# Kernel optimization log

Measured on AMD Instinct MI355X. Metric: run time of the kernel, lower is better.

The kernel has to match this reference:

```python
import jax, jax.numpy as jnp
import numpy as np
from jax import lax

B, S, H = 2, 2048, 768
FF = 1536
E = 8
TOP_K = 2


def setup_inputs() -> dict:
    key = jax.random.key(0)
    k1, k2, k3, k4 = jax.random.split(key, 4)
    hidden_states = jax.random.normal(k1, (B, S, H), dtype=jnp.float32)
    # torch init: weight.normal_() for experts; nn.Linear default init for gate (approx normal here is fine for a numerics baseline)
    gate_w = jax.random.normal(k2, (E, H), dtype=jnp.float32) * 0.02
    w_fc = jax.random.normal(k3, (E, FF, H), dtype=jnp.float32) * 0.02
    w_proj = jax.random.normal(k4, (E, H, FF), dtype=jnp.float32) * 0.02
    return {"hidden_states": hidden_states, "gate_w": gate_w, "w_fc": w_fc, "w_proj": w_proj}


def reference(hidden_states, gate_w, w_fc, w_proj):
    b, s, h = hidden_states.shape
    x = hidden_states.reshape(-1, h)                      # [T, H]
    # --- top-k gating (logits in float32, as in the torch code) ---
    logits = (x @ gate_w.T).astype(jnp.float32)           # [T, E]
    top_logits, top_idx = lax.top_k(logits, TOP_K)        # [T, K]
    gates = jax.nn.softmax(top_logits, axis=1).astype(x.dtype)  # [T, K]
    # combined per-token/per-expert gate: g[t,e] = sum_k gates[t,k]*[idx[t,k]==e]
    onehot = jax.nn.one_hot(top_idx, E, dtype=x.dtype)    # [T, K, E]
    g = jnp.einsum('tk,tke->te', gates, onehot)           # [T, E]
    # --- experts: gather + per-expert GEMM + gated scatter-add combine ---
    # Equivalent math: tokens with zero gate for expert e contribute nothing,
    # so compute each expert on all tokens and weight by g[:, e].
    out = jnp.zeros_like(x)
    for e in range(E):  # fixed small loop over experts (structurally distinct weights)
        hmid = jax.nn.gelu(x @ w_fc[e].T, approximate=False)   # [T, FF] (torch gelu = erf form)
        out = out + g[:, e:e + 1] * (hmid @ w_proj[e].T)       # [T, H]
    out = out.reshape(b, s, h)
    return out, logits
```

## Files before the change

### kernel.cpp

```cpp
#include <hip/hip_runtime.h>
#include <hip/hip_bf16.h>
#include <math.h>
#include <stdint.h>

#define TOKENS 4096
#define HDIM   768
#define FFDIM  1536
#define NEXP   8
#define NCT    12
#define WMAX   768
#define GEMM_GRID 768

typedef __attribute__((ext_vector_type(8))) short bf16x8;
typedef __attribute__((ext_vector_type(4))) float f32x4;

__device__ __forceinline__ unsigned short f2bf(float f) {
    union { float f; uint32_t u; } c; c.f = f;
    uint32_t u = c.u;
    uint32_t r = (u + 0x7FFFu + ((u >> 16) & 1u)) >> 16;
    return (unsigned short)r;
}

__device__ __forceinline__ void gload_lds16(const void* g, void* l) {
    __builtin_amdgcn_global_load_lds(
        (const __attribute__((address_space(1))) void*)g,
        (__attribute__((address_space(3))) void*)l, 16, 0, 0);
}

__global__ void cast_bf16_2(const float* __restrict__ s1, unsigned short* __restrict__ d1,
                            const float* __restrict__ s2, unsigned short* __restrict__ d2,
                            int n4) {
    int stride = gridDim.x * blockDim.x;
    for (int i = blockIdx.x * blockDim.x + threadIdx.x; i < 2 * n4; i += stride) {
        const float4* s = (i < n4) ? (const float4*)s1 : (const float4*)s2;
        ushort4* d = (i < n4) ? (ushort4*)d1 : (ushort4*)d2;
        int j = (i < n4) ? i : i - n4;
        float4 v = s[j];
        ushort4 o;
        o.x = f2bf(v.x); o.y = f2bf(v.y); o.z = f2bf(v.z); o.w = f2bf(v.w);
        d[j] = o;
    }
}

__global__ __launch_bounds__(256) void gating(
    const float* __restrict__ x, const float* __restrict__ gw,
    float* __restrict__ logits,
    int* __restrict__ tok_e, float* __restrict__ tok_g,
    unsigned short* __restrict__ x_bf, float* __restrict__ outp)
{
    float4 zz = make_float4(0.f, 0.f, 0.f, 0.f);
#pragma unroll
    for (int j = 0; j < 3; j++)
        ((float4*)outp)[blockIdx.x * 768 + j * 256 + threadIdx.x] = zz;

    int t = blockIdx.x * 4 + (threadIdx.x >> 6);
    int lane = threadIdx.x & 63;
    const float4* xt = (const float4*)(x + (size_t)t * HDIM);
    const float4* gw4 = (const float4*)gw;
    ushort4* xbt = (ushort4*)(x_bf + (size_t)t * HDIM);
    float acc[NEXP];
#pragma unroll
    for (int e = 0; e < NEXP; e++) acc[e] = 0.f;
#pragma unroll
    for (int it = 0; it < 3; it++) {
        int i = lane + it * 64;
        float4 xv = xt[i];
        ushort4 o;
        o.x = f2bf(xv.x); o.y = f2bf(xv.y); o.z = f2bf(xv.z); o.w = f2bf(xv.w);
        xbt[i] = o;
#pragma unroll
        for (int e = 0; e < NEXP; e++) {
            float4 wv = gw4[e * 192 + i];
            acc[e] += xv.x * wv.x + xv.y * wv.y + xv.z * wv.z + xv.w * wv.w;
        }
    }
#pragma unroll
    for (int e = 0; e < NEXP; e++) {
#pragma unroll
        for (int off = 32; off > 0; off >>= 1)
            acc[e] += __shfl_xor(acc[e], off);
    }
    if (lane == 0) {
        float4 l0 = make_float4(acc[0], acc[1], acc[2], acc[3]);
        float4 l1 = make_float4(acc[4], acc[5], acc[6], acc[7]);
        float4* lp = (float4*)(logits + (size_t)t * NEXP);
        lp[0] = l0; lp[1] = l1;
        int i0 = 0; float v0 = acc[0];
#pragma unroll
        for (int e = 1; e < NEXP; e++) if (acc[e] > v0) { v0 = acc[e]; i0 = e; }
        int i1 = -1; float v1 = -3.4e38f;
#pragma unroll
        for (int e = 0; e < NEXP; e++) if (e != i0 && acc[e] > v1) { v1 = acc[e]; i1 = e; }
        float g0 = 1.f / (1.f + expf(v1 - v0));
        tok_e[t * 2] = i0; tok_e[t * 2 + 1] = i1;
        tok_g[t * 2] = g0; tok_g[t * 2 + 1] = 1.f - g0;
    }
}

__global__ __launch_bounds__(1024) void build_lists(
    const int* __restrict__ tok_e, const float* __restrict__ tok_g,
    int* __restrict__ counts, int* __restrict__ bases, int* __restrict__ fill,
    int* __restrict__ work,
    int* __restrict__ entries, float* __restrict__ gates)
{
    __shared__ unsigned long long wlo[16], whi[16];
    __shared__ int scnt[8];
    int tid = threadIdx.x;
    int lane = tid & 63, wid = tid >> 6;

    int eL[8]; float gL[8];
    int4 ea = ((const int4*)tok_e)[tid * 2];
    int4 eb = ((const int4*)tok_e)[tid * 2 + 1];
    float4 ga = ((const float4*)tok_g)[tid * 2];
    float4 gb = ((const float4*)tok_g)[tid * 2 + 1];
    eL[0] = ea.x; eL[1] = ea.y; eL[2] = ea.z; eL[3] = ea.w;
    eL[4] = eb.x; eL[5] = eb.y; eL[6] = eb.z; eL[7] = eb.w;
    gL[0] = ga.x; gL[1] = ga.y; gL[2] = ga.z; gL[3] = ga.w;
    gL[4] = gb.x; gL[5] = gb.y; gL[6] = gb.z; gL[7] = gb.w;

    unsigned long long clo = 0, chi = 0;
#pragma unroll
    for (int j = 0; j < 8; j++) {
        int e = eL[j];
        unsigned long long one = 1ull << ((e & 3) * 16);
        if (e < 4) clo += one; else chi += one;
    }
    unsigned long long ilo = clo, ihi = chi;
#pragma unroll
    for (int s = 1; s < 64; s <<= 1) {
        unsigned long long t1 = __shfl_up(ilo, s);
        unsigned long long t2 = __shfl_up(ihi, s);
        if (lane >= s) { ilo += t1; ihi += t2; }
    }
    if (lane == 63) { wlo[wid] = ilo; whi[wid] = ihi; }
    __syncthreads();
    if (tid == 0) {
        unsigned long long rl = 0, rh = 0;
#pragma unroll
        for (int i = 0; i < 16; i++) {
            unsigned long long a = wlo[i], b = whi[i];
            wlo[i] = rl; whi[i] = rh;
            rl += a; rh += b;
        }
        int c[8];
#pragma unroll
        for (int e = 0; e < 4; e++) {
            c[e]     = (int)((rl >> (e * 16)) & 0xFFFF);
            c[e + 4] = (int)((rh >> (e * 16)) & 0xFFFF);
        }
        int b = 0;
#pragma unroll
        for (int e = 0; e < NEXP; e++) {
            scnt[e] = c[e]; counts[e] = c[e]; bases[e] = b; b += c[e];
            fill[e] = ((c[e] + 127) >> 7) * NCT;
        }
    }
    __syncthreads();
    if (tid < NEXP * NCT) {
        int e = tid / NCT, ct = tid % NCT;
        int rts = (scnt[e] + 127) >> 7;
        for (int r = 0; r < rts; r++)
            work[(ct * rts + r) * 8 + e] = (ct << 20) | (e << 16) | (r << 7);
    }
    unsigned long long rlo = wlo[wid] + (ilo - clo);
    unsigned long long rhi = whi[wid] + (ihi - chi);
#pragma unroll
    for (int j = 0; j < 8; j++) {
        int e = eL[j];
        int sh = (e & 3) * 16;
        unsigned long long one = 1ull << sh;
        int slot;
        if (e < 4) { slot = (int)((rlo >> sh) & 0xFFFF); rlo += one; }
        else       { slot = (int)((rhi >> sh) & 0xFFFF); rhi += one; }
        entries[e * TOKENS + slot] = tid * 8 + j;
        gates[e * TOKENS + slot]   = gL[j];
    }
}

template<int KD, int ND, int TN, bool IS_FC>
__global__ __launch_bounds__(256) void moe_gemm(
    const unsigned short* __restrict__ Asrc,
    const unsigned short* __restrict__ Bsrc,
    const int* __restrict__ counts,
    const int* __restrict__ bases,
    const int* __restrict__ fill,
    const int* __restrict__ work,
    const int* __restrict__ entries,
    const float* __restrict__ gates,
    unsigned short* __restrict__ hmid,
    float* __restrict__ outp)
{
    constexpr int AJ = TN / 32;
    constexpr int CB = TN / 32;
    int bkt = blockIdx.x & 7;
    int nfill = fill[bkt];

    int tid = threadIdx.x;
    int w = tid >> 6;
    int l = tid & 63;
    int sg = l & 7;
    int lr8 = l >> 3;
    int lo = l & 15;
    int q  = l >> 4;
    int wr = w >> 1, wc = w & 1;

    __shared__ __align__(16) unsigned short sA[128 * 64];
    __shared__ __align__(16) unsigned short sB[TN * 64];

    int aOff[4][2], bOff[AJ][2];
#pragma unroll
    for (int i = 0; i < 4; i++) {
        int m = wr * 64 + i * 16 + lo;
#pragma unroll
        for (int s = 0; s < 2; s++)
            aOff[i][s] = m * 64 + ((s * 4 + q) ^ (m & 7)) * 8;
    }
#pragma unroll
    for (int j = 0; j < AJ; j++) {
        int n = wc * (TN / 2) + j * 16 + lo;
#pragma unroll
        for (int s = 0; s < 2; s++)
            bOff[j][s] = n * 64 + ((s * 4 + q) ^ (n & 7)) * 8;
    }

    for (int p = blockIdx.x >> 3; p < nfill; p += GEMM_GRID / 8) {
        int pk   = work[p * 8 + bkt];
        int ct   = pk >> 20;
        int e    = (pk >> 16) & 0xF;
        int row0 = pk & 0xFFFF;
        int n_e  = counts[e];
        int ebase = bases[e];
        int n0 = ct * TN;
        const int* lst = entries + e * TOKENS;

        const unsigned short* Ag[4];
        int aLds[4];
#pragma unroll
        for (int c = 0; c < 4; c++) {
            int rr = w * 32 + c * 8 + lr8;
            int gr = row0 + rr;
            int id = gr < n_e ? gr : n_e - 1;
            size_t arow = IS_FC ? (size_t)(lst[id] >> 1) : (size_t)(ebase + id);
            Ag[c] = Asrc + arow * KD + (size_t)((sg ^ (rr & 7)) * 8);
            aLds[c] = (w * 32 + c * 8) * 64;
        }
        const unsigned short* Bg[CB];
        int bLds[CB];
#pragma unroll
        for (int c = 0; c < CB; c++) {
            int rr = w * (TN / 4) + c * 8 + lr8;
            Bg[c] = Bsrc + ((size_t)e * ND + n0 + rr) * KD + (size_t)((sg ^ (rr & 7)) * 8);
            bLds[c] = (w * (TN / 4) + c * 8) * 64;
        }

        f32x4 acc[4][AJ];
#pragma unroll
        for (int i = 0; i < 4; i++)
#pragma unroll
            for (int j = 0; j < AJ; j++) acc[i][j] = (f32x4){0.f, 0.f, 0.f, 0.f};

        for (int k0 = 0; k0 < KD; k0 += 64) {
#pragma unroll
            for (int c = 0; c < 4; c++) gload_lds16(Ag[c] + k0, sA + aLds[c]);
#pragma unroll
            for (int c = 0; c < CB; c++) gload_lds16(Bg[c] + k0, sB + bLds[c]);
            __syncthreads();
#pragma unroll
            for (int s = 0; s < 2; s++) {
                bf16x8 a[4], b[AJ];
#pragma unroll
                for (int i = 0; i < 4; i++) a[i] = *(const bf16x8*)(sA + aOff[i][s]);
#pragma unroll
                for (int j = 0; j < AJ; j++) b[j] = *(const bf16x8*)(sB + bOff[j][s]);
#pragma unroll
                for (int i = 0; i < 4; i++)
#pragma unroll
                    for (int j = 0; j < AJ; j++)
                        acc[i][j] = __builtin_amdgcn_mfma_f32_16x16x32_bf16(a[i], b[j], acc[i][j], 0, 0, 0);
            }
            __syncthreads();
        }

#pragma unroll
        for (int i = 0; i < 4; i++) {
            int rowB = row0 + wr * 64 + i * 16 + q * 4;
#pragma unroll
            for (int rr = 0; rr < 4; rr++) {
                int orow = rowB + rr;
                if (orow < n_e) {
                    if (IS_FC) {
                        size_t hrow = (size_t)(ebase + orow);
#pragma unroll
                        for (int j = 0; j < AJ; j++) {
                            float v = acc[i][j][rr];
                            v = 0.5f * v * (1.f + erff(v * 0.70710678118654752f));
                            hmid[hrow * ND + n0 + wc * (TN / 2) + j * 16 + lo] = f2bf(v);
                        }
                    } else {
                        int token = lst[orow] >> 1;
                        float g = gates[e * TOKENS + orow];
#pragma unroll
                        for (int j = 0; j < AJ; j++) {
                            atomicAdd(&outp[(size_t)token * ND + n0 + wc * (TN / 2) + j * 16 + lo],
                                      acc[i][j][rr] * g);
                        }
                    }
                }
            }
        }
    }
}

extern "C" void kernel_launch(void* const* d_in, const int* in_sizes, int n_in,
                              void* d_out, int out_size, void* d_ws, size_t ws_size,
                              hipStream_t stream) {
    const float* x     = (const float*)d_in[0];
    const float* gw    = (const float*)d_in[1];
    const float* wfc   = (const float*)d_in[2];
    const float* wproj = (const float*)d_in[3];
    float* outp   = (float*)d_out;
    float* logits = outp + (size_t)TOKENS * HDIM;

    char* ws = (char*)d_ws;
    int*   counts  = (int*)ws;
    int*   bases   = (int*)(ws + 64);
    int*   fill    = (int*)(ws + 128);
    int*   work    = (int*)(ws + 256);
    size_t off = 256 + (size_t)WMAX * 8 * 4;
    int*   entries = (int*)(ws + off);
    float* gates   = (float*)(ws + off + NEXP * TOKENS * 4);
    off += 2ull * NEXP * TOKENS * 4;
    int*   tok_e   = (int*)(ws + off);   off += (size_t)TOKENS * 2 * 4;
    float* tok_g   = (float*)(ws + off); off += (size_t)TOKENS * 2 * 4;
    unsigned short* x_bf   = (unsigned short*)(ws + off); off += (size_t)TOKENS * HDIM * 2;
    unsigned short* wfc_bf = (unsigned short*)(ws + off); off += (size_t)NEXP * FFDIM * HDIM * 2;
    unsigned short* wpj_bf = (unsigned short*)(ws + off); off += (size_t)NEXP * HDIM * FFDIM * 2;
    unsigned short* hmid   = (unsigned short*)(ws + off);

    cast_bf16_2<<<2048, 256, 0, stream>>>(wfc, wfc_bf, wproj, wpj_bf,
                                          NEXP * FFDIM * HDIM / 4);
    gating<<<TOKENS / 4, 256, 0, stream>>>(x, gw, logits, tok_e, tok_g, x_bf, outp);
    build_lists<<<1, 1024, 0, stream>>>(tok_e, tok_g, counts, bases, fill, work,
                                        entries, gates);
    moe_gemm<HDIM, FFDIM, 128, true ><<<GEMM_GRID, 256, 0, stream>>>(
        x_bf, wfc_bf, counts, bases, fill, work, entries, gates, hmid, outp);
    moe_gemm<FFDIM, HDIM, 64, false><<<GEMM_GRID, 256, 0, stream>>>(
        hmid, wpj_bf, counts, bases, fill, work, entries, gates, hmid, outp);
}
```

Before: 234.5 us.

## Double-buffer LDS tiles in MoE GEMM with 32-wide K stages

Splits each 64-wide K step into two 32-wide halves held in ping-pong LDS buffers, so the global-to-LDS load of the next half is issued before the MFMA work on the current one. The LDS swizzle and the per-thread load mapping are changed to match the 32-column tile layout. The aim is to hide global load latency behind compute. The cost is twice as many barriers per K step and more LDS per block, which could lower occupancy.

```diff
diff --git a/kernel.cpp b/kernel.cpp
--- a/kernel.cpp
+++ b/kernel.cpp
@@ -8,7 +8,6 @@
 #define FFDIM  1536
 #define NEXP   8
 #define NCT    12
-#define WMAX   768
 #define GEMM_GRID 768
 
 typedef __attribute__((ext_vector_type(8))) short bf16x8;
@@ -191,36 +190,55 @@
     float* __restrict__ outp)
 {
     constexpr int AJ = TN / 32;
-    constexpr int CB = TN / 32;
+    constexpr int CB = TN / 64;
     int bkt = blockIdx.x & 7;
     int nfill = fill[bkt];
 
     int tid = threadIdx.x;
     int w = tid >> 6;
     int l = tid & 63;
-    int sg = l & 7;
-    int lr8 = l >> 3;
+    int p4  = l & 3;
+    int lr16 = l >> 2;
     int lo = l & 15;
     int q  = l >> 4;
     int wr = w >> 1, wc = w & 1;
 
-    __shared__ __align__(16) unsigned short sA[128 * 64];
-    __shared__ __align__(16) unsigned short sB[TN * 64];
-
-    int aOff[4][2], bOff[AJ][2];
+    __shared__ __align__(16) unsigned short sA0[128 * 32], sA1[128 * 32];
+    __shared__ __align__(16) unsigned short sB0[TN * 32],  sB1[TN * 32];
+
+    int aOff[4], bOff[AJ];
 #pragma unroll
     for (int i = 0; i < 4; i++) {
         int m = wr * 64 + i * 16 + lo;
-#pragma unroll
-        for (int s = 0; s < 2; s++)
-            aOff[i][s] = m * 64 + ((s * 4 + q) ^ (m & 7)) * 8;
+        aOff[i] = m * 32 + (q ^ ((m >> 1) & 3)) * 8;
     }
 #pragma unroll
     for (int j = 0; j < AJ; j++) {
         int n = wc * (TN / 2) + j * 16 + lo;
-#pragma unroll
-        for (int s = 0; s < 2; s++)
-            bOff[j][s] = n * 64 + ((s * 4 + q) ^ (n & 7)) * 8;
+        bOff[j] = n * 32 + (q ^ ((n >> 1) & 3)) * 8;
+    }
+
+#define STAGE(kk, dA, dB)                                                     \
+    {                                                                         \
+        _Pragma("unroll")                                                     \
+        for (int c = 0; c < 2; c++)  gload_lds16(Ag[c] + (kk), (dA) + aLds[c]); \
+        _Pragma("unroll")                                                     \
+        for (int c = 0; c < CB; c++) gload_lds16(Bg[c] + (kk), (dB) + bLds[c]); \
+    }
+
+#define COMPUTE(sAb, sBb)                                                     \
+    {                                                                         \
+        bf16x8 a[4], b[AJ];                                                   \
+        _Pragma("unroll")                                                     \
+        for (int i = 0; i < 4; i++) a[i] = *(const bf16x8*)((sAb) + aOff[i]); \
+        _Pragma("unroll")                                                     \
+        for (int j = 0; j < AJ; j++) b[j] = *(const bf16x8*)((sBb) + bOff[j]); \
+        _Pragma("unroll")                                                     \
+        for (int i = 0; i < 4; i++)                                           \
+            _Pragma("unroll")                                                 \
+            for (int j = 0; j < AJ; j++)                                      \
+                acc[i][j] = __builtin_amdgcn_mfma_f32_16x16x32_bf16(          \
+                    a[i], b[j], acc[i][j], 0, 0, 0);                          \
     }
 
     for (int p = blockIdx.x >> 3; p < nfill; p += GEMM_GRID / 8) {
@@ -233,24 +251,24 @@
         int n0 = ct * TN;
         const int* lst = entries + e * TOKENS;
 
-        const unsigned short* Ag[4];
-        int aLds[4];
-#pragma unroll
-        for (int c = 0; c < 4; c++) {
-            int rr = w * 32 + c * 8 + lr8;
+        const unsigned short* Ag[2];
+        int aLds[2];
+#pragma unroll
+        for (int c = 0; c < 2; c++) {
+            int rr = w * 32 + c * 16 + lr16;
             int gr = row0 + rr;
             int id = gr < n_e ? gr : n_e - 1;
             size_t arow = IS_FC ? (size_t)(lst[id] >> 1) : (size_t)(ebase + id);
-            Ag[c] = Asrc + arow * KD + (size_t)((sg ^ (rr & 7)) * 8);
-            aLds[c] = (w * 32 + c * 8) * 64;
+            Ag[c] = Asrc + arow * KD + (size_t)((p4 ^ ((rr >> 1) & 3)) * 8);
+            aLds[c] = (w * 32 + c * 16) * 32;
         }
         const unsigned short* Bg[CB];
         int bLds[CB];
 #pragma unroll
         for (int c = 0; c < CB; c++) {
-            int rr = w * (TN / 4) + c * 8 + lr8;
-            Bg[c] = Bsrc + ((size_t)e * ND + n0 + rr) * KD + (size_t)((sg ^ (rr & 7)) * 8);
-            bLds[c] = (w * (TN / 4) + c * 8) * 64;
+            int rr = w * (TN / 4) + c * 16 + lr16;
+            Bg[c] = Bsrc + ((size_t)e * ND + n0 + rr) * KD + (size_t)((p4 ^ ((rr >> 1) & 3)) * 8);
+            bLds[c] = (w * (TN / 4) + c * 16) * 32;
         }
 
         f32x4 acc[4][AJ];
@@ -259,25 +277,14 @@
 #pragma unroll
             for (int j = 0; j < AJ; j++) acc[i][j] = (f32x4){0.f, 0.f, 0.f, 0.f};
 
+        STAGE(0, sA0, sB0);
+        __syncthreads();
         for (int k0 = 0; k0 < KD; k0 += 64) {
-#pragma unroll
-            for (int c = 0; c < 4; c++) gload_lds16(Ag[c] + k0, sA + aLds[c]);
-#pragma unroll
-            for (int c = 0; c < CB; c++) gload_lds16(Bg[c] + k0, sB + bLds[c]);
+            if (k0 + 32 < KD) STAGE(k0 + 32, sA1, sB1);
+            COMPUTE(sA0, sB0);
             __syncthreads();
-#pragma unroll
-            for (int s = 0; s < 2; s++) {
-                bf16x8 a[4], b[AJ];
-#pragma unroll
-                for (int i = 0; i < 4; i++) a[i] = *(const bf16x8*)(sA + aOff[i][s]);
-#pragma unroll
-                for (int j = 0; j < AJ; j++) b[j] = *(const bf16x8*)(sB + bOff[j][s]);
-#pragma unroll
-                for (int i = 0; i < 4; i++)
-#pragma unroll
-                    for (int j = 0; j < AJ; j++)
-                        acc[i][j] = __builtin_amdgcn_mfma_f32_16x16x32_bf16(a[i], b[j], acc[i][j], 0, 0, 0);
-            }
+            if (k0 + 64 < KD) STAGE(k0 + 64, sA0, sB0);
+            COMPUTE(sA1, sB1);
             __syncthreads();
         }
 
@@ -309,6 +316,8 @@
             }
         }
     }
+#undef STAGE
+#undef COMPUTE
 }
 
 extern "C" void kernel_launch(void* const* d_in, const int* in_sizes, int n_in,
@@ -326,7 +335,7 @@
     int*   bases   = (int*)(ws + 64);
     int*   fill    = (int*)(ws + 128);
     int*   work    = (int*)(ws + 256);
-    size_t off = 256 + (size_t)WMAX * 8 * 4;
+    size_t off = 256 + (size_t)768 * 8 * 4;
     int*   entries = (int*)(ws + off);
     float* gates   = (float*)(ws + off + NEXP * TOKENS * 4);
     off += 2ull * NEXP * TOKENS * 4;
```

Measured after the change: 248.9 us. 1.06x slower.

## Fuse fp32-to-bf16 weight conversion into MoE GEMM loads with register double buffering

Applied to the files above, without the earlier changes.

Drops the separate kernel that casts both expert weight tensors to bf16. The GEMMs now read fp32 weights directly and convert them in registers before writing to LDS. The direct global-to-LDS loads are replaced by register-staged loads with a two-stage software pipeline, so the next k-tile is fetched while the current one is computed. This removes a full read and write pass over the weights, but each weight tile is re-read in fp32 (twice the bytes) by every tile that uses it. It also adds register pressure and extra barriers per iteration.

```diff
diff --git a/kernel.cpp b/kernel.cpp
--- a/kernel.cpp
+++ b/kernel.cpp
@@ -8,7 +8,6 @@
 #define FFDIM  1536
 #define NEXP   8
 #define NCT    12
-#define WMAX   768
 #define GEMM_GRID 768
 
 typedef __attribute__((ext_vector_type(8))) short bf16x8;
@@ -21,25 +20,13 @@
     return (unsigned short)r;
 }
 
-__device__ __forceinline__ void gload_lds16(const void* g, void* l) {
-    __builtin_amdgcn_global_load_lds(
-        (const __attribute__((address_space(1))) void*)g,
-        (__attribute__((address_space(3))) void*)l, 16, 0, 0);
-}
-
-__global__ void cast_bf16_2(const float* __restrict__ s1, unsigned short* __restrict__ d1,
-                            const float* __restrict__ s2, unsigned short* __restrict__ d2,
-                            int n4) {
-    int stride = gridDim.x * blockDim.x;
-    for (int i = blockIdx.x * blockDim.x + threadIdx.x; i < 2 * n4; i += stride) {
-        const float4* s = (i < n4) ? (const float4*)s1 : (const float4*)s2;
-        ushort4* d = (i < n4) ? (ushort4*)d1 : (ushort4*)d2;
-        int j = (i < n4) ? i : i - n4;
-        float4 v = s[j];
-        ushort4 o;
-        o.x = f2bf(v.x); o.y = f2bf(v.y); o.z = f2bf(v.z); o.w = f2bf(v.w);
-        d[j] = o;
-    }
+__device__ __forceinline__ bf16x8 cvt8(float4 a, float4 b) {
+    union { bf16x8 v; __hip_bfloat162 p[4]; } u;
+    u.p[0] = __float22bfloat162_rn(make_float2(a.x, a.y));
+    u.p[1] = __float22bfloat162_rn(make_float2(a.z, a.w));
+    u.p[2] = __float22bfloat162_rn(make_float2(b.x, b.y));
+    u.p[3] = __float22bfloat162_rn(make_float2(b.z, b.w));
+    return u.v;
 }
 
 __global__ __launch_bounds__(256) void gating(
@@ -180,7 +167,7 @@
 template<int KD, int ND, int TN, bool IS_FC>
 __global__ __launch_bounds__(256) void moe_gemm(
     const unsigned short* __restrict__ Asrc,
-    const unsigned short* __restrict__ Bsrc,
+    const float* __restrict__ Bsrc,
     const int* __restrict__ counts,
     const int* __restrict__ bases,
     const int* __restrict__ fill,
@@ -190,16 +177,16 @@
     unsigned short* __restrict__ hmid,
     float* __restrict__ outp)
 {
-    constexpr int AJ = TN / 32;
-    constexpr int CB = TN / 32;
+    constexpr int AJ   = TN / 32;
+    constexpr int BSEG = TN / 32;
     int bkt = blockIdx.x & 7;
     int nfill = fill[bkt];
 
     int tid = threadIdx.x;
     int w = tid >> 6;
     int l = tid & 63;
-    int sg = l & 7;
-    int lr8 = l >> 3;
+    int gs  = tid & 7;
+    int rg  = tid >> 3;
     int lo = l & 15;
     int q  = l >> 4;
     int wr = w >> 1, wc = w & 1;
@@ -221,6 +208,42 @@
 #pragma unroll
         for (int s = 0; s < 2; s++)
             bOff[j][s] = n * 64 + ((s * 4 + q) ^ (n & 7)) * 8;
+    }
+
+#define LOADR(st, kk)                                                         \
+    {                                                                         \
+        _Pragma("unroll")                                                     \
+        for (int c = 0; c < 4; c++) rA[st][c] = *(const bf16x8*)(Ap[c] + (kk)); \
+        _Pragma("unroll")                                                     \
+        for (int c = 0; c < BSEG; c++) {                                      \
+            rB[st][c][0] = *(const float4*)(Bp[c] + (kk));                    \
+            rB[st][c][1] = *(const float4*)(Bp[c] + (kk) + 4);                \
+        }                                                                     \
+    }
+#define WRITE(st)                                                             \
+    {                                                                         \
+        _Pragma("unroll")                                                     \
+        for (int c = 0; c < 4; c++) *(bf16x8*)(sA + aW[c]) = rA[st][c];       \
+        _Pragma("unroll")                                                     \
+        for (int c = 0; c < BSEG; c++)                                        \
+            *(bf16x8*)(sB + bW[c]) = cvt8(rB[st][c][0], rB[st][c][1]);        \
+    }
+#define COMPUTE                                                               \
+    {                                                                         \
+        _Pragma("unroll")                                                     \
+        for (int s = 0; s < 2; s++) {                                         \
+            bf16x8 a[4], b[AJ];                                               \
+            _Pragma("unroll")                                                 \
+            for (int i = 0; i < 4; i++) a[i] = *(const bf16x8*)(sA + aOff[i][s]); \
+            _Pragma("unroll")                                                 \
+            for (int j = 0; j < AJ; j++) b[j] = *(const bf16x8*)(sB + bOff[j][s]); \
+            _Pragma("unroll")                                                 \
+            for (int i = 0; i < 4; i++)                                       \
+                _Pragma("unroll")                                             \
+                for (int j = 0; j < AJ; j++)                                  \
+                    acc[i][j] = __builtin_amdgcn_mfma_f32_16x16x32_bf16(      \
+                        a[i], b[j], acc[i][j], 0, 0, 0);                      \
+        }                                                                     \
     }
 
     for (int p = blockIdx.x >> 3; p < nfill; p += GEMM_GRID / 8) {
@@ -233,24 +256,22 @@
         int n0 = ct * TN;
         const int* lst = entries + e * TOKENS;
 
-        const unsigned short* Ag[4];
-        int aLds[4];
+        const unsigned short* Ap[4]; int aW[4];
 #pragma unroll
         for (int c = 0; c < 4; c++) {
-            int rr = w * 32 + c * 8 + lr8;
+            int rr = rg * 4 + c;
             int gr = row0 + rr;
             int id = gr < n_e ? gr : n_e - 1;
             size_t arow = IS_FC ? (size_t)(lst[id] >> 1) : (size_t)(ebase + id);
-            Ag[c] = Asrc + arow * KD + (size_t)((sg ^ (rr & 7)) * 8);
-            aLds[c] = (w * 32 + c * 8) * 64;
-        }
-        const unsigned short* Bg[CB];
-        int bLds[CB];
-#pragma unroll
-        for (int c = 0; c < CB; c++) {
-            int rr = w * (TN / 4) + c * 8 + lr8;
-            Bg[c] = Bsrc + ((size_t)e * ND + n0 + rr) * KD + (size_t)((sg ^ (rr & 7)) * 8);
-            bLds[c] = (w * (TN / 4) + c * 8) * 64;
+            Ap[c] = Asrc + arow * KD + gs * 8;
+            aW[c] = rr * 64 + (gs ^ (rr & 7)) * 8;
+        }
+        const float* Bp[BSEG]; int bW[BSEG];
+#pragma unroll
+        for (int c = 0; c < BSEG; c++) {
+            int rr = rg * BSEG + c;
+            Bp[c] = Bsrc + ((size_t)e * ND + n0 + rr) * KD + gs * 8;
+            bW[c] = rr * 64 + (gs ^ (rr & 7)) * 8;
         }
 
         f32x4 acc[4][AJ];
@@ -259,25 +280,20 @@
 #pragma unroll
             for (int j = 0; j < AJ; j++) acc[i][j] = (f32x4){0.f, 0.f, 0.f, 0.f};
 
-        for (int k0 = 0; k0 < KD; k0 += 64) {
-#pragma unroll
-            for (int c = 0; c < 4; c++) gload_lds16(Ag[c] + k0, sA + aLds[c]);
-#pragma unroll
-            for (int c = 0; c < CB; c++) gload_lds16(Bg[c] + k0, sB + bLds[c]);
+        bf16x8 rA[2][4];
+        float4 rB[2][BSEG][2];
+
+        LOADR(0, 0);
+        for (int k0 = 0; k0 < KD; k0 += 128) {
+            if (k0 + 64 < KD) LOADR(1, k0 + 64);
+            WRITE(0);
             __syncthreads();
-#pragma unroll
-            for (int s = 0; s < 2; s++) {
-                bf16x8 a[4], b[AJ];
-#pragma unroll
-                for (int i = 0; i < 4; i++) a[i] = *(const bf16x8*)(sA + aOff[i][s]);
-#pragma unroll
-                for (int j = 0; j < AJ; j++) b[j] = *(const bf16x8*)(sB + bOff[j][s]);
-#pragma unroll
-                for (int i = 0; i < 4; i++)
-#pragma unroll
-                    for (int j = 0; j < AJ; j++)
-                        acc[i][j] = __builtin_amdgcn_mfma_f32_16x16x32_bf16(a[i], b[j], acc[i][j], 0, 0, 0);
-            }
+            COMPUTE;
+            __syncthreads();
+            if (k0 + 128 < KD) LOADR(0, k0 + 128);
+            WRITE(1);
+            __syncthreads();
+            COMPUTE;
             __syncthreads();
         }
 
@@ -309,6 +325,9 @@
             }
         }
     }
+#undef LOADR
+#undef WRITE
+#undef COMPUTE
 }
 
 extern "C" void kernel_launch(void* const* d_in, const int* in_sizes, int n_in,
@@ -326,24 +345,20 @@
     int*   bases   = (int*)(ws + 64);
     int*   fill    = (int*)(ws + 128);
     int*   work    = (int*)(ws + 256);
-    size_t off = 256 + (size_t)WMAX * 8 * 4;
+    size_t off = 256 + (size_t)768 * 8 * 4;
     int*   entries = (int*)(ws + off);
     float* gates   = (float*)(ws + off + NEXP * TOKENS * 4);
     off += 2ull * NEXP * TOKENS * 4;
     int*   tok_e   = (int*)(ws + off);   off += (size_t)TOKENS * 2 * 4;
     float* tok_g   = (float*)(ws + off); off += (size_t)TOKENS * 2 * 4;
-    unsigned short* x_bf   = (unsigned short*)(ws + off); off += (size_t)TOKENS * HDIM * 2;
-    unsigned short* wfc_bf = (unsigned short*)(ws + off); off += (size_t)NEXP * FFDIM * HDIM * 2;
-    unsigned short* wpj_bf = (unsigned short*)(ws + off); off += (size_t)NEXP * HDIM * FFDIM * 2;
-    unsigned short* hmid   = (unsigned short*)(ws + off);
-
-    cast_bf16_2<<<2048, 256, 0, stream>>>(wfc, wfc_bf, wproj, wpj_bf,
-                                          NEXP * FFDIM * HDIM / 4);
+    unsigned short* x_bf = (unsigned short*)(ws + off); off += (size_t)TOKENS * HDIM * 2;
+    unsigned short* hmid = (unsigned short*)(ws + off);
+
     gating<<<TOKENS / 4, 256, 0, stream>>>(x, gw, logits, tok_e, tok_g, x_bf, outp);
     build_lists<<<1, 1024, 0, stream>>>(tok_e, tok_g, counts, bases, fill, work,
                                         entries, gates);
     moe_gemm<HDIM, FFDIM, 128, true ><<<GEMM_GRID, 256, 0, stream>>>(
-        x_bf, wfc_bf, counts, bases, fill, work, entries, gates, hmid, outp);
+        x_bf, wfc, counts, bases, fill, work, entries, gates, hmid, outp);
     moe_gemm<FFDIM, HDIM, 64, false><<<GEMM_GRID, 256, 0, stream>>>(
-        hmid, wpj_bf, counts, bases, fill, work, entries, gates, hmid, outp);
-}
+        hmid, wproj, counts, bases, fill, work, entries, gates, hmid, outp);
+}
```

After: 283.6 us. +20.9%, slower.

## Switch MoE GEMM to independent per-wave 64x64 tiles with wave-local sync

Applied to the files above, without the earlier changes.

Restructures the expert GEMMs so that each wave owns its own 64x64 output tile and its own LDS slice, with a K step of 32. Block-wide __syncthreads are replaced by a per-wave vmem waitcnt drain. Work lists are rebuilt for 64-row tiles, giving separate fc and proj lists with 24 and 12 column tiles. The aim is to remove block-level barrier stalls and padding waste on 128-row tiles, and to raise occupancy with launch_bounds(256,3). In exchange, operand reuse drops because each wave loads its own A and B with no sharing, and double buffering is absent, so each wave stalls on its own load before its MFMAs.

```diff
diff --git a/kernel.cpp b/kernel.cpp
--- a/kernel.cpp
+++ b/kernel.cpp
@@ -7,8 +7,8 @@
 #define HDIM   768
 #define FFDIM  1536
 #define NEXP   8
-#define NCT    12
-#define WMAX   768
+#define NCTA   24
+#define NCTB   12
 #define GEMM_GRID 768
 
 typedef __attribute__((ext_vector_type(8))) short bf16x8;
@@ -25,6 +25,11 @@
     __builtin_amdgcn_global_load_lds(
         (const __attribute__((address_space(1))) void*)g,
         (__attribute__((address_space(3))) void*)l, 16, 0, 0);
+}
+
+__device__ __forceinline__ void wave_vmem_drain() {
+    __builtin_amdgcn_s_waitcnt(0x0F70);
+    asm volatile("" ::: "memory");
 }
 
 __global__ void cast_bf16_2(const float* __restrict__ s1, unsigned short* __restrict__ d1,
@@ -99,8 +104,9 @@
 
 __global__ __launch_bounds__(1024) void build_lists(
     const int* __restrict__ tok_e, const float* __restrict__ tok_g,
-    int* __restrict__ counts, int* __restrict__ bases, int* __restrict__ fill,
-    int* __restrict__ work,
+    int* __restrict__ counts, int* __restrict__ bases,
+    int* __restrict__ fillA, int* __restrict__ fillB,
+    int* __restrict__ workA, int* __restrict__ workB,
     int* __restrict__ entries, float* __restrict__ gates)
 {
     __shared__ unsigned long long wlo[16], whi[16];
@@ -152,15 +158,24 @@
 #pragma unroll
         for (int e = 0; e < NEXP; e++) {
             scnt[e] = c[e]; counts[e] = c[e]; bases[e] = b; b += c[e];
-            fill[e] = ((c[e] + 127) >> 7) * NCT;
+            int rts = (c[e] + 63) >> 6;
+            fillA[e] = rts * NCTA;
+            fillB[e] = rts * NCTB;
         }
     }
     __syncthreads();
-    if (tid < NEXP * NCT) {
-        int e = tid / NCT, ct = tid % NCT;
-        int rts = (scnt[e] + 127) >> 7;
+    if (tid < NEXP * NCTA) {
+        int e = tid / NCTA, ct = tid % NCTA;
+        int rts = (scnt[e] + 63) >> 6;
         for (int r = 0; r < rts; r++)
-            work[(ct * rts + r) * 8 + e] = (ct << 20) | (e << 16) | (r << 7);
+            workA[(ct * rts + r) * 8 + e] = (ct << 20) | (e << 16) | (r << 6);
+    }
+    if (tid >= 256 && tid < 256 + NEXP * NCTB) {
+        int t2 = tid - 256;
+        int e = t2 / NCTB, ct = t2 % NCTB;
+        int rts = (scnt[e] + 63) >> 6;
+        for (int r = 0; r < rts; r++)
+            workB[(ct * rts + r) * 8 + e] = (ct << 20) | (e << 16) | (r << 6);
     }
     unsigned long long rlo = wlo[wid] + (ilo - clo);
     unsigned long long rhi = whi[wid] + (ihi - chi);
@@ -177,8 +192,8 @@
     }
 }
 
-template<int KD, int ND, int TN, bool IS_FC>
-__global__ __launch_bounds__(256) void moe_gemm(
+template<int KD, int ND, bool IS_FC>
+__global__ __launch_bounds__(256, 3) void moe_gemm(
     const unsigned short* __restrict__ Asrc,
     const unsigned short* __restrict__ Bsrc,
     const int* __restrict__ counts,
@@ -190,100 +205,80 @@
     unsigned short* __restrict__ hmid,
     float* __restrict__ outp)
 {
-    constexpr int AJ = TN / 32;
-    constexpr int CB = TN / 32;
     int bkt = blockIdx.x & 7;
     int nfill = fill[bkt];
 
     int tid = threadIdx.x;
     int w = tid >> 6;
     int l = tid & 63;
-    int sg = l & 7;
-    int lr8 = l >> 3;
+    int p4  = l & 3;
+    int lr16 = l >> 2;
     int lo = l & 15;
     int q  = l >> 4;
-    int wr = w >> 1, wc = w & 1;
-
-    __shared__ __align__(16) unsigned short sA[128 * 64];
-    __shared__ __align__(16) unsigned short sB[TN * 64];
-
-    int aOff[4][2], bOff[AJ][2];
+
+    __shared__ __align__(16) unsigned short sA[4 * 64 * 32];
+    __shared__ __align__(16) unsigned short sB[4 * 64 * 32];
+    unsigned short* sAq = sA + w * 2048;
+    unsigned short* sBq = sB + w * 2048;
+
+    int aOff[4], bOff[4];
 #pragma unroll
     for (int i = 0; i < 4; i++) {
-        int m = wr * 64 + i * 16 + lo;
-#pragma unroll
-        for (int s = 0; s < 2; s++)
-            aOff[i][s] = m * 64 + ((s * 4 + q) ^ (m & 7)) * 8;
-    }
-#pragma unroll
-    for (int j = 0; j < AJ; j++) {
-        int n = wc * (TN / 2) + j * 16 + lo;
-#pragma unroll
-        for (int s = 0; s < 2; s++)
-            bOff[j][s] = n * 64 + ((s * 4 + q) ^ (n & 7)) * 8;
-    }
-
-    for (int p = blockIdx.x >> 3; p < nfill; p += GEMM_GRID / 8) {
+        int m = i * 16 + lo;
+        aOff[i] = m * 32 + (q ^ ((m >> 1) & 3)) * 8;
+        bOff[i] = aOff[i];
+    }
+
+    for (int p = (blockIdx.x >> 3) * 4 + w; p < nfill; p += (GEMM_GRID / 8) * 4) {
         int pk   = work[p * 8 + bkt];
         int ct   = pk >> 20;
         int e    = (pk >> 16) & 0xF;
         int row0 = pk & 0xFFFF;
         int n_e  = counts[e];
         int ebase = bases[e];
-        int n0 = ct * TN;
+        int n0 = ct * 64;
         const int* lst = entries + e * TOKENS;
 
         const unsigned short* Ag[4];
-        int aLds[4];
+        const unsigned short* Bg[4];
 #pragma unroll
         for (int c = 0; c < 4; c++) {
-            int rr = w * 32 + c * 8 + lr8;
+            int rr = c * 16 + lr16;
             int gr = row0 + rr;
             int id = gr < n_e ? gr : n_e - 1;
             size_t arow = IS_FC ? (size_t)(lst[id] >> 1) : (size_t)(ebase + id);
-            Ag[c] = Asrc + arow * KD + (size_t)((sg ^ (rr & 7)) * 8);
-            aLds[c] = (w * 32 + c * 8) * 64;
-        }
-        const unsigned short* Bg[CB];
-        int bLds[CB];
-#pragma unroll
-        for (int c = 0; c < CB; c++) {
-            int rr = w * (TN / 4) + c * 8 + lr8;
-            Bg[c] = Bsrc + ((size_t)e * ND + n0 + rr) * KD + (size_t)((sg ^ (rr & 7)) * 8);
-            bLds[c] = (w * (TN / 4) + c * 8) * 64;
-        }
-
-        f32x4 acc[4][AJ];
+            int gseg = p4 ^ ((rr >> 1) & 3);
+            Ag[c] = Asrc + arow * KD + gseg * 8;
+            Bg[c] = Bsrc + ((size_t)e * ND + n0 + rr) * KD + gseg * 8;
+        }
+
+        f32x4 acc[4][4];
 #pragma unroll
         for (int i = 0; i < 4; i++)
 #pragma unroll
-            for (int j = 0; j < AJ; j++) acc[i][j] = (f32x4){0.f, 0.f, 0.f, 0.f};
-
-        for (int k0 = 0; k0 < KD; k0 += 64) {
-#pragma unroll
-            for (int c = 0; c < 4; c++) gload_lds16(Ag[c] + k0, sA + aLds[c]);
-#pragma unroll
-            for (int c = 0; c < CB; c++) gload_lds16(Bg[c] + k0, sB + bLds[c]);
-            __syncthreads();
-#pragma unroll
-            for (int s = 0; s < 2; s++) {
-                bf16x8 a[4], b[AJ];
-#pragma unroll
-                for (int i = 0; i < 4; i++) a[i] = *(const bf16x8*)(sA + aOff[i][s]);
-#pragma unroll
-                for (int j = 0; j < AJ; j++) b[j] = *(const bf16x8*)(sB + bOff[j][s]);
-#pragma unroll
-                for (int i = 0; i < 4; i++)
-#pragma unroll
-                    for (int j = 0; j < AJ; j++)
-                        acc[i][j] = __builtin_amdgcn_mfma_f32_16x16x32_bf16(a[i], b[j], acc[i][j], 0, 0, 0);
-            }
-            __syncthreads();
+            for (int j = 0; j < 4; j++) acc[i][j] = (f32x4){0.f, 0.f, 0.f, 0.f};
+
+        for (int k0 = 0; k0 < KD; k0 += 32) {
+#pragma unroll
+            for (int c = 0; c < 4; c++) gload_lds16(Ag[c] + k0, sAq + c * 512);
+#pragma unroll
+            for (int c = 0; c < 4; c++) gload_lds16(Bg[c] + k0, sBq + c * 512);
+            wave_vmem_drain();
+            bf16x8 a[4], b[4];
+#pragma unroll
+            for (int i = 0; i < 4; i++) a[i] = *(const bf16x8*)(sAq + aOff[i]);
+#pragma unroll
+            for (int j = 0; j < 4; j++) b[j] = *(const bf16x8*)(sBq + bOff[j]);
+#pragma unroll
+            for (int i = 0; i < 4; i++)
+#pragma unroll
+                for (int j = 0; j < 4; j++)
+                    acc[i][j] = __builtin_amdgcn_mfma_f32_16x16x32_bf16(a[i], b[j], acc[i][j], 0, 0, 0);
         }
 
 #pragma unroll
         for (int i = 0; i < 4; i++) {
-            int rowB = row0 + wr * 64 + i * 16 + q * 4;
+            int rowB = row0 + i * 16 + q * 4;
 #pragma unroll
             for (int rr = 0; rr < 4; rr++) {
                 int orow = rowB + rr;
@@ -291,17 +286,17 @@
                     if (IS_FC) {
                         size_t hrow = (size_t)(ebase + orow);
 #pragma unroll
-                        for (int j = 0; j < AJ; j++) {
+                        for (int j = 0; j < 4; j++) {
                             float v = acc[i][j][rr];
                             v = 0.5f * v * (1.f + erff(v * 0.70710678118654752f));
-                            hmid[hrow * ND + n0 + wc * (TN / 2) + j * 16 + lo] = f2bf(v);
+                            hmid[hrow * ND + n0 + j * 16 + lo] = f2bf(v);
                         }
                     } else {
                         int token = lst[orow] >> 1;
                         float g = gates[e * TOKENS + orow];
 #pragma unroll
-                        for (int j = 0; j < AJ; j++) {
-                            atomicAdd(&outp[(size_t)token * ND + n0 + wc * (TN / 2) + j * 16 + lo],
+                        for (int j = 0; j < 4; j++) {
+                            atomicAdd(&outp[(size_t)token * ND + n0 + j * 16 + lo],
                                       acc[i][j][rr] * g);
                         }
                     }
@@ -324,9 +319,11 @@
     char* ws = (char*)d_ws;
     int*   counts  = (int*)ws;
     int*   bases   = (int*)(ws + 64);
-    int*   fill    = (int*)(ws + 128);
-    int*   work    = (int*)(ws + 256);
-    size_t off = 256 + (size_t)WMAX * 8 * 4;
+    int*   fillA   = (int*)(ws + 128);
+    int*   fillB   = (int*)(ws + 192);
+    int*   workA   = (int*)(ws + 256);
+    size_t off = 256 + (size_t)3072 * 8 * 4;
+    int*   workB   = (int*)(ws + off); off += (size_t)1536 * 8 * 4;
     int*   entries = (int*)(ws + off);
     float* gates   = (float*)(ws + off + NEXP * TOKENS * 4);
     off += 2ull * NEXP * TOKENS * 4;
@@ -340,10 +337,10 @@
     cast_bf16_2<<<2048, 256, 0, stream>>>(wfc, wfc_bf, wproj, wpj_bf,
                                           NEXP * FFDIM * HDIM / 4);
     gating<<<TOKENS / 4, 256, 0, stream>>>(x, gw, logits, tok_e, tok_g, x_bf, outp);
-    build_lists<<<1, 1024, 0, stream>>>(tok_e, tok_g, counts, bases, fill, work,
-                                        entries, gates);
-    moe_gemm<HDIM, FFDIM, 128, true ><<<GEMM_GRID, 256, 0, stream>>>(
-        x_bf, wfc_bf, counts, bases, fill, work, entries, gates, hmid, outp);
-    moe_gemm<FFDIM, HDIM, 64, false><<<GEMM_GRID, 256, 0, stream>>>(
-        hmid, wpj_bf, counts, bases, fill, work, entries, gates, hmid, outp);
-}
+    build_lists<<<1, 1024, 0, stream>>>(tok_e, tok_g, counts, bases, fillA, fillB,
+                                        workA, workB, entries, gates);
+    moe_gemm<HDIM, FFDIM, true ><<<GEMM_GRID, 256, 0, stream>>>(
+        x_bf, wfc_bf, counts, bases, fillA, workA, entries, gates, hmid, outp);
+    moe_gemm<FFDIM, HDIM, false><<<GEMM_GRID, 256, 0, stream>>>(
+        hmid, wpj_bf, counts, bases, fillB, workB, entries, gates, hmid, outp);
+}
```

Measured after the change: 243.6 us. +3.9%, slower.
